# Kernel optimization log

Measured on AMD Instinct MI355X. Metric: run time of the kernel, lower is better.

## Reference

```python
import jax, jax.numpy as jnp
import numpy as np
from jax import lax

POST_NMS_TOP_N = 1000   # cfg[cfg_key].RPN_POST_NMS_TOP_N
NMS_THRESH = 0.7        # cfg[cfg_key].RPN_NMS_THRESH
NEG = -1e9
B, N = 4, 65536


def setup_inputs() -> dict:
    key = jax.random.key(0)
    k0, k1, k2, k3, k4, k5, k6 = jax.random.split(key, 7)
    scores = jax.random.uniform(k0, (B, N), dtype=jnp.float32)
    # small deltas so exp(dw) stays in a realistic range
    bbox_deltas = 0.1 * jax.random.normal(k1, (B, N, 4), dtype=jnp.float32)
    # plausible anchor boxes inside a 1024x1024 image
    cx = jax.random.uniform(k2, (N,), minval=0.0, maxval=1024.0)
    cy = jax.random.uniform(k3, (N,), minval=0.0, maxval=1024.0)
    w = jax.random.uniform(k4, (N,), minval=16.0, maxval=256.0)
    h = jax.random.uniform(k5, (N,), minval=16.0, maxval=256.0)
    anchors = jnp.stack([cx - 0.5 * w, cy - 0.5 * h, cx + 0.5 * w, cy + 0.5 * h], axis=-1).astype(jnp.float32)
    im_info = jnp.tile(jnp.array([[1024.0, 1024.0, 1.0]], dtype=jnp.float32), (B, 1))
    ids = jax.random.randint(k6, (N,), 0, 5, dtype=jnp.int32)  # FPN level ids
    return {"scores": scores, "bbox_deltas": bbox_deltas, "anchors": anchors,
            "im_info": im_info, "ids": ids}


def _iou_one(box, boxes):
    # box [4], boxes [N,4]; mmcv convention (no +1)
    x1 = jnp.maximum(box[0], boxes[:, 0])
    y1 = jnp.maximum(box[1], boxes[:, 1])
    x2 = jnp.minimum(box[2], boxes[:, 2])
    y2 = jnp.minimum(box[3], boxes[:, 3])
    inter = jnp.clip(x2 - x1, 0.0) * jnp.clip(y2 - y1, 0.0)
    a1 = (box[2] - box[0]) * (box[3] - box[1])
    a2 = (boxes[:, 2] - boxes[:, 0]) * (boxes[:, 3] - boxes[:, 1])
    return inter / jnp.maximum(a1 + a2 - inter, 1e-6)


def _nms_single(boxes, scores, ids):
    # batched_nms: offset boxes by level id so levels never suppress each other
    max_c = jnp.max(boxes) + 1.0
    boxes_off = boxes + (ids.astype(boxes.dtype) * max_c)[:, None]

    def step(s, _):
        i = jnp.argmax(s)
        valid = s[i] > NEG * 0.5
        iou = _iou_one(boxes_off[i], boxes_off)
        s_new = jnp.where(iou > NMS_THRESH, NEG, s).at[i].set(NEG)
        sel = jnp.where(valid, boxes[i], jnp.zeros((4,), boxes.dtype))
        return s_new, sel

    _, sel = lax.scan(step, scores, None, length=POST_NMS_TOP_N)
    return sel  # [POST_NMS_TOP_N, 4], in descending score order (as batched_nms returns)


def _forward(scores, bbox_deltas, anchors, im_info, ids):
    ws = anchors[:, 2] - anchors[:, 0] + 1.0          # [N]
    hs = anchors[:, 3] - anchors[:, 1] + 1.0
    ctr_x = anchors[:, 0] + 0.5 * ws
    ctr_y = anchors[:, 1] + 0.5 * hs
    dx, dy, dw, dh = (bbox_deltas[..., 0], bbox_deltas[..., 1],
                      bbox_deltas[..., 2], bbox_deltas[..., 3])  # [B,N]
    pcx = dx * ws + ctr_x
    pcy = dy * hs + ctr_y
    pw = jnp.exp(dw) * ws
    ph = jnp.exp(dh) * hs
    proposals = jnp.stack([pcx - 0.5 * pw, pcy - 0.5 * ph,
                           pcx + 0.5 * pw, pcy + 0.5 * ph], axis=-1)  # [B,N,4]
    # clip_boxes: x in [0, w-1], y in [0, h-1]
    wmax = im_info[:, 1][:, None] - 1.0
    hmax = im_info[:, 0][:, None] - 1.0
    x1 = jnp.clip(proposals[..., 0], 0.0, wmax)
    y1 = jnp.clip(proposals[..., 1], 0.0, hmax)
    x2 = jnp.clip(proposals[..., 2], 0.0, wmax)
    y2 = jnp.clip(proposals[..., 3], 0.0, hmax)
    proposals = jnp.stack([x1, y1, x2, y2], axis=-1)
    # per-image batched NMS (greedy descending-score selection == sort + NMS)
    sel = jax.vmap(_nms_single, in_axes=(0, 0, None))(proposals, scores, ids)  # [B,topN,4]
    batch_col = jnp.broadcast_to(
        jnp.arange(scores.shape[0], dtype=sel.dtype)[:, None, None],
        (scores.shape[0], POST_NMS_TOP_N, 1))
    return jnp.concatenate([batch_col, sel], axis=-1)  # [B,topN,5]


def reference(scores, bbox_deltas, anchors, im_info, ids):
    return _forward(scores, bbox_deltas, anchors, im_info, ids)
```

## Files before the change

### kernel.cpp

```cpp
#include <hip/hip_runtime.h>
#include <stdint.h>

#define NB     65536
#define BATCH  4
#define TOPN   1000
#define MMAX   2048
#define NTILE  (MMAX / 64)
#define NPAIRS (NTILE * (NTILE + 1) / 2)
#define CAP    128
#define KSUP   8
#define UNC    128
#define THRESH 0.974f
#define NEGV   (-1e9f)
#define NMS_T  0.7f
#define GRIDN  256

#define OFF_CBLK   64
#define OFF_KRAW   1088
#define OFF_SBOX   263232
#define OFF_SLEV   394304
#define OFF_CNT2   427072
#define OFF_SUP    459840
#define OFF_BAR    721984

__device__ __forceinline__ void st_u32(uint32_t* p, uint32_t v) {
  __hip_atomic_store(p, v, __ATOMIC_RELAXED, __HIP_MEMORY_SCOPE_AGENT);
}
__device__ __forceinline__ uint32_t ld_u32(const uint32_t* p) {
  return __hip_atomic_load((uint32_t*)p, __ATOMIC_RELAXED, __HIP_MEMORY_SCOPE_AGENT);
}
__device__ __forceinline__ void st_u64(unsigned long long* p, unsigned long long v) {
  __hip_atomic_store(p, v, __ATOMIC_RELAXED, __HIP_MEMORY_SCOPE_AGENT);
}
__device__ __forceinline__ unsigned long long ld_u64(const unsigned long long* p) {
  return __hip_atomic_load((unsigned long long*)p, __ATOMIC_RELAXED,
                           __HIP_MEMORY_SCOPE_AGENT);
}
__device__ __forceinline__ void st_f4(float4* p, float4 v) {
  union { float4 f; unsigned long long u[2]; } c; c.f = v;
  st_u64((unsigned long long*)p, c.u[0]);
  st_u64((unsigned long long*)p + 1, c.u[1]);
}
__device__ __forceinline__ float4 ld_f4(const float4* p) {
  union { float4 f; unsigned long long u[2]; } c;
  c.u[0] = ld_u64((const unsigned long long*)p);
  c.u[1] = ld_u64((const unsigned long long*)p + 1);
  return c.f;
}

__device__ __forceinline__ void decode_box(const float4* __restrict__ anchors4,
                                           const float4* __restrict__ deltas4,
                                           int b, int i, float wmax, float hmax,
                                           float& x1, float& y1, float& x2, float& y2) {
  float4 a = anchors4[i];
  float4 d = deltas4[(size_t)b * NB + i];
  float ws = a.z - a.x + 1.0f;
  float hs = a.w - a.y + 1.0f;
  float cx = a.x + 0.5f * ws;
  float cy = a.y + 0.5f * hs;
  float pcx = d.x * ws + cx;
  float pcy = d.y * hs + cy;
  float pw = expf(d.z) * ws;
  float ph = expf(d.w) * hs;
  x1 = pcx - 0.5f * pw; y1 = pcy - 0.5f * ph;
  x2 = pcx + 0.5f * pw; y2 = pcy + 0.5f * ph;
  x1 = fminf(fmaxf(x1, 0.0f), wmax);
  y1 = fminf(fmaxf(y1, 0.0f), hmax);
  x2 = fminf(fmaxf(x2, 0.0f), wmax);
  y2 = fminf(fmaxf(y2, 0.0f), hmax);
}

__device__ __forceinline__ uint32_t blockscan(uint32_t v, volatile uint32_t* wsum,
                                              int tid, uint32_t* total) {
  __syncthreads();
  int lane = tid & 63, wid = tid >> 6;
  uint32_t x = v;
  for (int off = 1; off < 64; off <<= 1) {
    uint32_t u = __shfl_up(x, off, 64);
    if (lane >= off) x += u;
  }
  if (lane == 63) wsum[wid] = x;
  __syncthreads();
  if (tid == 0) {
    uint32_t run = 0;
    for (int w = 0; w < 4; ++w) { uint32_t t = wsum[w]; wsum[w] = run; run += t; }
    wsum[4] = run;
  }
  __syncthreads();
  *total = wsum[4];
  return x - v + wsum[wid];
}

__device__ __forceinline__ void gbar(uint32_t* bar, int bid, int tid, uint32_t g) {
  __syncthreads();
  if (tid == 0) {
    const uint32_t tgt = g + 1u;
    uint32_t* slot = bar + (bid & 15) * 16;
    uint32_t* root = bar + 16 * 16;
    uint32_t* mir  = bar + (17 + (bid & 7)) * 16;
    uint32_t a = __hip_atomic_fetch_add(slot, 1u, __ATOMIC_RELAXED, __HIP_MEMORY_SCOPE_AGENT);
    if (a == 15u) {
      uint32_t r = __hip_atomic_fetch_add(root, 1u, __ATOMIC_RELAXED, __HIP_MEMORY_SCOPE_AGENT);
      if (r == 15u) {
        __hip_atomic_store(root, 0u, __ATOMIC_RELAXED, __HIP_MEMORY_SCOPE_AGENT);
        for (int s = 0; s < 16; ++s)
          __hip_atomic_store(bar + s * 16, 0u, __ATOMIC_RELAXED, __HIP_MEMORY_SCOPE_AGENT);
        asm volatile("s_waitcnt vmcnt(0)" ::: "memory");
        for (int m = 0; m < 8; ++m)
          __hip_atomic_fetch_add(bar + (17 + m) * 16, 1u, __ATOMIC_RELAXED,
                                 __HIP_MEMORY_SCOPE_AGENT);
      }
    }
    while (__hip_atomic_load(mir, __ATOMIC_RELAXED, __HIP_MEMORY_SCOPE_AGENT) < tgt)
      __builtin_amdgcn_s_sleep(4);
  }
  __syncthreads();
}

__global__ void k_init(uint32_t* bar) {
  if (threadIdx.x < 25)
    __hip_atomic_store(&bar[threadIdx.x * 16], 0u, __ATOMIC_RELAXED,
                       __HIP_MEMORY_SCOPE_AGENT);
}

__global__ __launch_bounds__(256) void k_fused(
    const float* __restrict__ scores, const float4* __restrict__ deltas4,
    const float4* __restrict__ anchors4, const float* __restrict__ im_info,
    const int* __restrict__ ids,
    unsigned long long* __restrict__ keys_raw, uint32_t* __restrict__ cnt_blk,
    uint32_t* ctrs, float4* __restrict__ sboxes, int* __restrict__ slev,
    uint32_t* __restrict__ cnt2, int* __restrict__ suplist,
    uint32_t* __restrict__ bar, float* __restrict__ out) {
  const int bid = blockIdx.x;
  const int tid = threadIdx.x;
  const int lane = tid & 63, wid = tid >> 6;

  __shared__ uint32_t wsum[17];
  __shared__ unsigned long long sk[MMAX];
  __shared__ uint32_t scnt[64], sbs[64];
  __shared__ uint32_t psum[256];
  __shared__ uint32_t meta[2];
  __shared__ uint8_t  kept[MMAX];
  __shared__ uint16_t unc[UNC];
  __shared__ int      supld[UNC][KSUP];
  __shared__ uint8_t  supn[UNC];
  __shared__ uint16_t unr[UNC];
  __shared__ uint32_t mask[NB / 32];
  __shared__ float    rv[256];
  __shared__ int      ri[256];
  __shared__ float    fm[4];

  {
    const int b = bid >> 6;
    const int blk = bid & 63;
    const float4* s4 = (const float4*)scores + (size_t)b * (NB / 4) + (size_t)blk * 256 + tid;
    float4 s = *s4;
    float sc4[4] = {s.x, s.y, s.z, s.w};
    uint32_t cmask = 0, ccount = 0;
#pragma unroll
    for (int k = 0; k < 4; ++k)
      if (sc4[k] >= THRESH) { cmask |= (1u << k); ccount++; }
    uint32_t total;
    uint32_t p = blockscan(ccount, wsum, tid, &total);
    if (tid == 0) st_u32(&cnt_blk[bid], total);
    unsigned long long* dst = keys_raw + (size_t)bid * CAP;
#pragma unroll
    for (int k = 0; k < 4; ++k) {
      if (cmask & (1u << k)) {
        if (p < (uint32_t)CAP) {
          int i = (blk << 10) + (tid << 2) + k;
          st_u64(&dst[p],
                 ((unsigned long long)(~__float_as_uint(sc4[k])) << 32) | (uint32_t)i);
        }
        p++;
      }
    }
  }

  gbar(bar, bid, tid, 0u);

  if (bid < NTILE * BATCH) {
    const int b = bid >> 5;
    const int r = bid & 31;
    if (tid < 64) {
      uint32_t c = ld_u32(&cnt_blk[b * 64 + tid]);
      uint32_t cc = min(c, (uint32_t)CAP);
      scnt[tid] = cc;
      uint32_t x = cc;
      for (int off = 1; off < 64; off <<= 1) {
        uint32_t u = __shfl_up(x, off, 64);
        if (lane >= off) x += u;
      }
      sbs[tid] = x - cc;
      unsigned long long ov = __ballot(c > (uint32_t)CAP);
      if (tid == 63) { meta[0] = x; meta[1] = (ov != 0ULL) ? 1u : 0u; }
    }
    __syncthreads();
    uint32_t nsum = meta[0];
    int n = min((int)nsum, MMAX);
    uint32_t flag = meta[1] | ((nsum > (uint32_t)MMAX) ? 1u : 0u);
    if (r == 0 && tid == 0) {
      st_u32(&ctrs[b], (uint32_t)n);
      st_u32(&ctrs[8 + b], flag);
    }
    if (tid < 64) st_u32(&cnt2[(size_t)b * MMAX + r * 64 + tid], 0u);
    {
      int k = tid >> 2, q = tid & 3;
      uint32_t cb = sbs[k], cc = scnt[k];
      const unsigned long long* src = keys_raw + ((size_t)b * 64 + k) * CAP;
      for (uint32_t o0 = q; o0 < cc; o0 += 32) {
        unsigned long long v[8];
#pragma unroll
        for (int u = 0; u < 8; ++u) {
          uint32_t o = o0 + 4u * u;
          if (o < cc) v[u] = ld_u64(&src[o]);
        }
#pragma unroll
        for (int u = 0; u < 8; ++u) {
          uint32_t o = o0 + 4u * u;
          uint32_t d = cb + o;
          if (o < cc && d < (uint32_t)MMAX) sk[d] = v[u];
        }
      }
    }
    for (int i = tid; i < MMAX; i += 256) if (i >= n) sk[i] = ~0ULL;
    __syncthreads();
    int c = r * 64 + lane;
    uint32_t partial = 0;
    if (c < n) {
      unsigned long long myk = sk[c];
      const ulonglong2* p2 = (const ulonglong2*)(sk + (size_t)wid * 512);
      for (int it = 0; it < 256; it += 4) {
        ulonglong2 a = p2[it], bq = p2[it + 1], cq = p2[it + 2], dq = p2[it + 3];
        partial += (uint32_t)(a.x < myk) + (uint32_t)(a.y < myk) +
                   (uint32_t)(bq.x < myk) + (uint32_t)(bq.y < myk) +
                   (uint32_t)(cq.x < myk) + (uint32_t)(cq.y < myk) +
                   (uint32_t)(dq.x < myk) + (uint32_t)(dq.y < myk);
      }
    }
    psum[wid * 64 + lane] = partial;
    __syncthreads();
    if (tid < 64) {
      int cc = r * 64 + tid;
      if (cc < n) {
        uint32_t rank = psum[tid] + psum[64 + tid] + psum[128 + tid] + psum[192 + tid];
        if (rank < (uint32_t)MMAX) {
          unsigned long long key = sk[cc];
          int i = (int)(uint32_t)key;
          float wmax = im_info[b * 3 + 1] - 1.0f;
          float hmax = im_info[b * 3 + 0] - 1.0f;
          float x1, y1, x2, y2;
          decode_box(anchors4, deltas4, b, i, wmax, hmax, x1, y1, x2, y2);
          st_f4(&sboxes[(size_t)b * MMAX + rank], make_float4(x1, y1, x2, y2));
          st_u32((uint32_t*)&slev[(size_t)b * MMAX + rank], (uint32_t)ids[i]);
        }
      }
    }
  }

  gbar(bar, bid, tid, 1u);

  {
    const int gwid = bid * 4 + wid;
    for (int t = gwid; t < NPAIRS * BATCH; t += 1024) {
      const int b = t & 3;
      const int p = t >> 2;
      int tj = (int)((sqrtf(8.0f * (float)p + 1.0f) - 1.0f) * 0.5f);
      while ((tj + 1) * (tj + 2) / 2 <= p) ++tj;
      while (tj * (tj + 1) / 2 > p) --tj;
      int ti = p - tj * (tj + 1) / 2;
      int n = min((int)ld_u32(&ctrs[b]), MMAX);
      if (tj * 64 >= n) continue;

      int ii = ti * 64 + lane;
      float4 I = make_float4(0.f, 0.f, 0.f, 0.f);
      int ilv = -1;
      if (ii < n) {
        I = ld_f4(&sboxes[(size_t)b * MMAX + ii]);
        ilv = (int)ld_u32((const uint32_t*)&slev[(size_t)b * MMAX + ii]);
      }
      int j = tj * 64 + lane;
      bool jv = (j < n);
      float4 J = make_float4(0.f, 0.f, 0.f, 0.f);
      int jl = -2;
      float aj = 0.0f;
      if (jv) {
        J = ld_f4(&sboxes[(size_t)b * MMAX + j]);
        jl = (int)ld_u32((const uint32_t*)&slev[(size_t)b * MMAX + j]);
        aj = (J.z - J.x) * (J.w - J.y);
      }
      int imax = (ti == tj) ? lane : 64;
      for (int k = 0; k < 64; ++k) {
        int   kl = __shfl(ilv, k, 64);
        float Ix = __shfl(I.x, k, 64);
        float Iy = __shfl(I.y, k, 64);
        float Iz = __shfl(I.z, k, 64);
        float Iw = __shfl(I.w, k, 64);
        if (!jv || k >= imax || kl != jl) continue;
        float xx1 = fmaxf(Ix, J.x), yy1 = fmaxf(Iy, J.y);
        float xx2 = fminf(Iz, J.z), yy2 = fminf(Iw, J.w);
        float inter = fmaxf(xx2 - xx1, 0.0f) * fmaxf(yy2 - yy1, 0.0f);
        float ai = (Iz - Ix) * (Iw - Iy);
        float iou = inter / fmaxf((ai + aj) - inter, 1e-6f);
        if (iou > NMS_T) {
          uint32_t s = atomicAdd(&cnt2[(size_t)b * MMAX + j], 1u);
          if (s < (uint32_t)KSUP)
            st_u32((uint32_t*)&suplist[((size_t)b * MMAX + j) * KSUP + s],
                   (uint32_t)(ti * 64 + k));
          else atomicOr(&ctrs[8 + b], 1u);
        }
      }
    }
  }

  gbar(bar, bid, tid, 2u);

  if (bid < BATCH) {
    const int b = bid;
    int n = min((int)ld_u32(&ctrs[b]), MMAX);
    const int jb = tid * 8;
    uint32_t cj[8];
    uint32_t uf = 0, usum = 0;
#pragma unroll
    for (int k = 0; k < 8; ++k) {
      int j = jb + k;
      uint32_t c = (j < n) ? ld_u32(&cnt2[(size_t)b * MMAX + j]) : 0u;
      cj[k] = c;
      kept[j] = (j < n && c == 0u) ? 1 : 0;
      uint32_t u = (j < n && c > 0u) ? 1u : 0u;
      uf |= (u << k); usum += u;
    }
    uint32_t tot_unc;
    uint32_t base = blockscan(usum, wsum, tid, &tot_unc);
    {
      uint32_t p = base;
#pragma unroll
      for (int k = 0; k < 8; ++k) {
        if ((uf >> k) & 1u) {
          if (p < (uint32_t)UNC) {
            int j = jb + k;
            int m = (int)min(cj[k], (uint32_t)KSUP);
            unc[p] = (uint16_t)j; supn[p] = (uint8_t)m;
            for (int s = 0; s < m; ++s)
              supld[p][s] = (int)ld_u32((const uint32_t*)&suplist[((size_t)b * MMAX + j) * KSUP + s]);
          }
          p++;
        }
      }
    }
    uint32_t nu32 = min(tot_unc, (uint32_t)UNC);
    for (int sw = 0; sw < 3; ++sw) {
      __syncthreads();
      if (tid < (int)nu32) {
        int j = unc[tid];
        if (kept[j] == 0) {
          int m = (int)supn[tid];
          bool anyK = false, allS = true;
          for (int s = 0; s < m; ++s) {
            uint8_t st = kept[supld[tid][s]];
            anyK |= (st == 1); allS &= (st == 2);
          }
          if (anyK) kept[j] = 2;
          else if (allS) kept[j] = 1;
        }
      }
    }
    __syncthreads();
    uint32_t isun = (tid < (int)nu32 && kept[unc[tid]] == 0) ? 1u : 0u;
    uint32_t nunr_tot;
    uint32_t upos = blockscan(isun, wsum, tid, &nunr_tot);
    if (isun) unr[upos] = (uint16_t)tid;
    __syncthreads();
    if (tid < 64) {
      int nr = (int)nunr_tot;
      for (int u2 = 0; u2 < nr; ++u2) {
        int u = unr[u2];
        int m = (int)supn[u];
        int pred = (tid < m) ? ((kept[supld[u][tid]] == 1) ? 1 : 0) : 0;
        unsigned long long bal = __ballot(pred);
        if (tid == 0) kept[unc[u]] = (bal == 0ULL) ? 1 : 2;
      }
    }
    __syncthreads();
    uint32_t kf = 0, ksum = 0;
#pragma unroll
    for (int k = 0; k < 8; ++k) {
      uint32_t kk = (kept[jb + k] == 1) ? 1u : 0u;
      kf |= (kk << k); ksum += kk;
    }
    uint32_t total;
    uint32_t pb = blockscan(ksum, wsum, tid, &total);
    {
      uint32_t p = pb;
#pragma unroll
      for (int k = 0; k < 8; ++k) {
        if ((kf >> k) & 1u) {
          if (p < (uint32_t)TOPN) {
            float4 bx = ld_f4(&sboxes[(size_t)b * MMAX + jb + k]);
            size_t o = ((size_t)b * TOPN + p) * 5;
            out[o] = (float)b; out[o+1] = bx.x; out[o+2] = bx.y; out[o+3] = bx.z; out[o+4] = bx.w;
          }
          p++;
        }
      }
    }
    for (int t = tid; t < TOPN; t += 256) {
      if ((uint32_t)t >= total) {
        size_t o = ((size_t)b * TOPN + t) * 5;
        out[o] = (float)b; out[o+1] = 0.0f; out[o+2] = 0.0f; out[o+3] = 0.0f; out[o+4] = 0.0f;
      }
    }

    bool needFB = (ld_u32(&ctrs[8 + b]) != 0u) || (total < (uint32_t)TOPN) ||
                  (tot_unc > (uint32_t)UNC);
    if (needFB) {
      const float wmax = im_info[b * 3 + 1] - 1.0f;
      const float hmax = im_info[b * 3 + 0] - 1.0f;
      __syncthreads();
      float mx = 0.0f;
      for (int i = tid; i < NB; i += 256) {
        float x1, y1, x2, y2;
        decode_box(anchors4, deltas4, b, i, wmax, hmax, x1, y1, x2, y2);
        mx = fmaxf(mx, fmaxf(fmaxf(x1, y1), fmaxf(x2, y2)));
      }
      for (int o = 32; o > 0; o >>= 1) mx = fmaxf(mx, __shfl_xor(mx, o, 64));
      if ((tid & 63) == 0) fm[tid >> 6] = mx;
      __syncthreads();
      if (tid == 0) fm[0] = fmaxf(fmaxf(fm[0], fm[1]), fmaxf(fm[2], fm[3]));
      for (int i = tid; i < NB / 32; i += 256) mask[i] = 0u;
      __syncthreads();
      float max_c = fm[0] + 1.0f;
      for (int it = 0; it < TOPN; ++it) {
        float bv = -3e38f; int bi = 0x7fffffff;
        for (int i = tid; i < NB; i += 256) {
          bool sup = (mask[i >> 5] >> (i & 31)) & 1u;
          float v = sup ? NEGV : scores[(size_t)b * NB + i];
          if (v > bv || (v == bv && i < bi)) { bv = v; bi = i; }
        }
        rv[tid] = bv; ri[tid] = bi;
        __syncthreads();
        for (int s = 128; s > 0; s >>= 1) {
          if (tid < s) {
            float v2 = rv[tid + s]; int i2 = ri[tid + s];
            if (v2 > rv[tid] || (v2 == rv[tid] && i2 < ri[tid])) { rv[tid] = v2; ri[tid] = i2; }
          }
          __syncthreads();
        }
        int ii = ri[0]; float vv = rv[0];
        bool valid = vv > NEGV * 0.5f;
        if (!valid) {
          if (tid == 0) {
            size_t o = ((size_t)b * TOPN + it) * 5;
            out[o] = (float)b; out[o+1] = 0; out[o+2] = 0; out[o+3] = 0; out[o+4] = 0;
          }
          __syncthreads();
          continue;
        }
        float x1, y1, x2, y2;
        decode_box(anchors4, deltas4, b, ii, wmax, hmax, x1, y1, x2, y2);
        int lv = ids[ii];
        float off = (float)lv * max_c;
        float s0 = x1 + off, s1 = y1 + off, s2 = x2 + off, s3 = y2 + off;
        float a1 = (s2 - s0) * (s3 - s1);
        if (tid == 0) {
          size_t o = ((size_t)b * TOPN + it) * 5;
          out[o] = (float)b; out[o+1] = x1; out[o+2] = y1; out[o+3] = x2; out[o+4] = y2;
        }
        for (int j = tid; j < NB; j += 256) {
          if ((mask[j >> 5] >> (j & 31)) & 1u) continue;
          if (ids[j] != lv) continue;
          float bx1, by1, bx2, by2;
          decode_box(anchors4, deltas4, b, j, wmax, hmax, bx1, by1, bx2, by2);
          float t0 = bx1 + off, t1 = by1 + off, t2 = bx2 + off, t3 = by2 + off;
          float xx1 = fmaxf(s0, t0), yy1 = fmaxf(s1, t1);
          float xx2 = fminf(s2, t2), yy2 = fminf(s3, t3);
          float inter = fmaxf(xx2 - xx1, 0.0f) * fmaxf(yy2 - yy1, 0.0f);
          float a2r = (t2 - t0) * (t3 - t1);
          float iou = inter / fmaxf(a1 + a2r - inter, 1e-6f);
          if (iou > NMS_T) atomicOr(&mask[j >> 5], 1u << (j & 31));
        }
        if (tid == 0) atomicOr(&mask[ii >> 5], 1u << (ii & 31));
        __syncthreads();
      }
    }
  }
}

extern "C" void kernel_launch(void* const* d_in, const int* in_sizes, int n_in,
                              void* d_out, int out_size, void* d_ws, size_t ws_size,
                              hipStream_t stream) {
  const float*  scores   = (const float*)d_in[0];
  const float4* deltas4  = (const float4*)d_in[1];
  const float4* anchors4 = (const float4*)d_in[2];
  const float*  im_info  = (const float*)d_in[3];
  const int*    ids      = (const int*)d_in[4];
  float* out = (float*)d_out;

  char* ws = (char*)d_ws;
  uint32_t*           ctrs     = (uint32_t*)ws;
  uint32_t*           cnt_blk  = (uint32_t*)(ws + OFF_CBLK);
  unsigned long long* keys_raw = (unsigned long long*)(ws + OFF_KRAW);
  float4*             sboxes   = (float4*)(ws + OFF_SBOX);
  int*                slev     = (int*)(ws + OFF_SLEV);
  uint32_t*           cnt2     = (uint32_t*)(ws + OFF_CNT2);
  int*                suplist  = (int*)(ws + OFF_SUP);
  uint32_t*           bar      = (uint32_t*)(ws + OFF_BAR);

  hipLaunchKernelGGL(k_init, dim3(1), dim3(64), 0, stream, bar);
  hipLaunchKernelGGL(k_fused, dim3(GRIDN), dim3(256), 0, stream,
                     scores, deltas4, anchors4, im_info, ids,
                     keys_raw, cnt_blk, ctrs, sboxes, slev, cnt2, suplist, bar, out);
}
```

Before: 112.9 us.

## Replace atomic tree grid barrier with flag-based master-polled barrier and early exit

The hierarchical atomic-counter grid barrier is replaced by a flag scheme: each block writes its own padded flag, one master block polls all 256 flags with a wavefront and then releases 8 mirror flags that the other blocks spin on. Blocks not needed for the final serial stage now post their flag and exit instead of waiting at the last barrier. Per-image counts are hoisted out of the pair loop, and suppressor lists are loaded unconditionally and unrolled. This removes atomic contention and reset traffic on the barrier path, at the cost of a single master-polling bottleneck and reliance on plain stores and loads for ordering.

New measurement: 114.7 us. No clear change (+1.6%).

```diff
diff --git a/kernel.cpp b/kernel.cpp
--- a/kernel.cpp
+++ b/kernel.cpp
@@ -91,35 +91,35 @@
   return x - v + wsum[wid];
 }
 
-__device__ __forceinline__ void gbar(uint32_t* bar, int bid, int tid, uint32_t g) {
+__device__ __forceinline__ void gbar(uint32_t* bar, int bid, int tid, uint32_t tgt) {
   __syncthreads();
-  if (tid == 0) {
-    const uint32_t tgt = g + 1u;
-    uint32_t* slot = bar + (bid & 15) * 16;
-    uint32_t* root = bar + 16 * 16;
-    uint32_t* mir  = bar + (17 + (bid & 7)) * 16;
-    uint32_t a = __hip_atomic_fetch_add(slot, 1u, __ATOMIC_RELAXED, __HIP_MEMORY_SCOPE_AGENT);
-    if (a == 15u) {
-      uint32_t r = __hip_atomic_fetch_add(root, 1u, __ATOMIC_RELAXED, __HIP_MEMORY_SCOPE_AGENT);
-      if (r == 15u) {
-        __hip_atomic_store(root, 0u, __ATOMIC_RELAXED, __HIP_MEMORY_SCOPE_AGENT);
-        for (int s = 0; s < 16; ++s)
-          __hip_atomic_store(bar + s * 16, 0u, __ATOMIC_RELAXED, __HIP_MEMORY_SCOPE_AGENT);
-        asm volatile("s_waitcnt vmcnt(0)" ::: "memory");
-        for (int m = 0; m < 8; ++m)
-          __hip_atomic_fetch_add(bar + (17 + m) * 16, 1u, __ATOMIC_RELAXED,
-                                 __HIP_MEMORY_SCOPE_AGENT);
-      }
-    }
-    while (__hip_atomic_load(mir, __ATOMIC_RELAXED, __HIP_MEMORY_SCOPE_AGENT) < tgt)
-      __builtin_amdgcn_s_sleep(4);
+  if (bid == GRIDN - 1) {
+    if (tid == 0) st_u32(bar + (size_t)bid * 16, tgt);
+    if (tid < 64) {
+      for (;;) {
+        bool ok = true;
+#pragma unroll
+        for (int r = 0; r < 4; ++r)
+          ok = ok && (ld_u32(bar + (size_t)(tid + r * 64) * 16) >= tgt);
+        if (__all(ok)) break;
+        __builtin_amdgcn_s_sleep(1);
+      }
+      if (tid < 8) st_u32(bar + (size_t)(256 + tid) * 16, tgt);
+    }
+  } else {
+    if (tid == 0) {
+      st_u32(bar + (size_t)bid * 16, tgt);
+      while (ld_u32(bar + (size_t)(256 + (bid & 7)) * 16) < tgt)
+        __builtin_amdgcn_s_sleep(2);
+    }
   }
   __syncthreads();
 }
 
 __global__ void k_init(uint32_t* bar) {
-  if (threadIdx.x < 25)
-    __hip_atomic_store(&bar[threadIdx.x * 16], 0u, __ATOMIC_RELAXED,
+  int t = threadIdx.x + blockIdx.x * 264;
+  if (t < 264)
+    __hip_atomic_store(&bar[(size_t)t * 16], 0u, __ATOMIC_RELAXED,
                        __HIP_MEMORY_SCOPE_AGENT);
 }
 
@@ -177,7 +177,7 @@
     }
   }
 
-  gbar(bar, bid, tid, 0u);
+  gbar(bar, bid, tid, 1u);
 
   if (bid < NTILE * BATCH) {
     const int b = bid >> 5;
@@ -258,9 +258,12 @@
     }
   }
 
-  gbar(bar, bid, tid, 1u);
+  gbar(bar, bid, tid, 2u);
 
   {
+    uint32_t nimg[BATCH];
+#pragma unroll
+    for (int b2 = 0; b2 < BATCH; ++b2) nimg[b2] = ld_u32(&ctrs[b2]);
     const int gwid = bid * 4 + wid;
     for (int t = gwid; t < NPAIRS * BATCH; t += 1024) {
       const int b = t & 3;
@@ -269,7 +272,7 @@
       while ((tj + 1) * (tj + 2) / 2 <= p) ++tj;
       while (tj * (tj + 1) / 2 > p) --tj;
       int ti = p - tj * (tj + 1) / 2;
-      int n = min((int)ld_u32(&ctrs[b]), MMAX);
+      int n = min((int)nimg[b], MMAX);
       if (tj * 64 >= n) continue;
 
       int ii = ti * 64 + lane;
@@ -313,9 +316,15 @@
     }
   }
 
-  gbar(bar, bid, tid, 2u);
-
-  if (bid < BATCH) {
+  if (bid >= BATCH && bid != GRIDN - 1) {
+    __syncthreads();
+    if (tid == 0) st_u32(bar + (size_t)bid * 16, 3u);
+    return;
+  }
+  gbar(bar, bid, tid, 3u);
+  if (bid >= BATCH) return;
+
+  {
     const int b = bid;
     int n = min((int)ld_u32(&ctrs[b]), MMAX);
     const int jb = tid * 8;
@@ -340,9 +349,12 @@
           if (p < (uint32_t)UNC) {
             int j = jb + k;
             int m = (int)min(cj[k], (uint32_t)KSUP);
+            uint32_t sl[KSUP];
+            const uint32_t* srow = (const uint32_t*)&suplist[((size_t)b * MMAX + j) * KSUP];
+#pragma unroll
+            for (int s = 0; s < KSUP; ++s) sl[s] = ld_u32(&srow[s]);
             unc[p] = (uint16_t)j; supn[p] = (uint8_t)m;
-            for (int s = 0; s < m; ++s)
-              supld[p][s] = (int)ld_u32((const uint32_t*)&suplist[((size_t)b * MMAX + j) * KSUP + s]);
+            for (int s = 0; s < m; ++s) supld[p][s] = (int)sl[s];
           }
           p++;
         }
@@ -506,7 +518,7 @@
   int*                suplist  = (int*)(ws + OFF_SUP);
   uint32_t*           bar      = (uint32_t*)(ws + OFF_BAR);
 
-  hipLaunchKernelGGL(k_init, dim3(1), dim3(64), 0, stream, bar);
+  hipLaunchKernelGGL(k_init, dim3(1), dim3(264), 0, stream, bar);
   hipLaunchKernelGGL(k_fused, dim3(GRIDN), dim3(256), 0, stream,
                      scores, deltas4, anchors4, im_info, ids,
                      keys_raw, cnt_blk, ctrs, sboxes, slev, cnt2, suplist, bar, out);
```
